# Optimization experiments

Hardware: AMD Instinct MI355X
Metric: run time of the kernel (lower is better)

The kernel has to match this reference:

```python
import jax, jax.numpy as jnp
import numpy as np

N = 10000
IN_DIM = 256
HID = 256
HEADS = 8
NUM_CLASSES = 40
EPS = 1e-5
NEG_SLOPE = 0.2


def gat_conv(x, src, dst, W, a_src, a_dst, bias, concat):
    # x: [N, F_in]; W: [F_in, H*C]; a_src/a_dst: [H, C]
    n = x.shape[0]
    H, C = a_src.shape
    h = (x @ W).reshape(n, H, C)                       # [N,H,C]
    s_src = jnp.einsum('nhc,hc->nh', h, a_src)         # [N,H]
    s_dst = jnp.einsum('nhc,hc->nh', h, a_dst)         # [N,H]
    score = jax.nn.leaky_relu(s_src[src] + s_dst[dst], NEG_SLOPE)  # [E,H]
    m = jax.lax.stop_gradient(jax.ops.segment_max(score, dst, num_segments=n))
    e = jnp.exp(score - m[dst])                        # [E,H]
    denom = jax.ops.segment_sum(e, dst, num_segments=n)
    alpha = e / denom[dst]                             # per-dst edge softmax
    msg = h[src] * alpha[:, :, None]                   # [E,H,C]
    out = jax.ops.segment_sum(msg, dst, num_segments=n)  # [N,H,C]
    out = out.reshape(n, H * C) if concat else out.mean(axis=1)
    return out + bias


def batch_norm(x, gamma, beta):
    mu = x.mean(axis=0)
    var = x.var(axis=0)
    return gamma * (x - mu) * jax.lax.rsqrt(var + EPS) + beta


def setup_inputs() -> dict:
    key = jax.random.key(0)
    ks = jax.random.split(key, 16)
    C0 = HID // HEADS  # 32, concat layer
    x = jax.random.normal(ks[0], (N, IN_DIM), jnp.float32)
    edge_index = jax.random.randint(ks[1], (2, 160000), 0, N, jnp.int32)
    def lin(k, fi, fo):
        return jax.random.normal(k, (fi, fo), jnp.float32) / np.sqrt(fi)
    return {
        'x': x,
        'edge_index': edge_index,
        'W0': lin(ks[2], IN_DIM, HEADS * C0),
        'a_src0': jax.random.normal(ks[3], (HEADS, C0), jnp.float32) * 0.1,
        'a_dst0': jax.random.normal(ks[4], (HEADS, C0), jnp.float32) * 0.1,
        'b0': jnp.zeros((HID,), jnp.float32),
        'g0': jnp.ones((HID,), jnp.float32),
        'be0': jnp.zeros((HID,), jnp.float32),
        'W1': lin(ks[5], HID, HEADS * HID),
        'a_src1': jax.random.normal(ks[6], (HEADS, HID), jnp.float32) * 0.1,
        'a_dst1': jax.random.normal(ks[7], (HEADS, HID), jnp.float32) * 0.1,
        'b1': jnp.zeros((HID,), jnp.float32),
        'g1': jnp.ones((HID,), jnp.float32),
        'be1': jnp.zeros((HID,), jnp.float32),
        'Wc': lin(ks[8], HID, NUM_CLASSES),
        'bc': jnp.zeros((NUM_CLASSES,), jnp.float32),
    }


def reference(x, edge_index, W0, a_src0, a_dst0, b0, g0, be0,
              W1, a_src1, a_dst1, b1, g1, be1, Wc, bc):
    n = x.shape[0]
    loops = jnp.arange(n, dtype=edge_index.dtype)
    src = jnp.concatenate([edge_index[0], loops])  # add_self_loops=True
    dst = jnp.concatenate([edge_index[1], loops])

    # layer 0: concat=True -> [N, 256]
    h = gat_conv(x, src, dst, W0, a_src0, a_dst0, b0, concat=True)
    h = jax.nn.elu(batch_norm(h, g0, be0))
    # i==0: no residual; dropout is identity at eval

    # layer 1 (last): concat=False (mean over heads) -> [N, 256]
    h_in = h
    h = gat_conv(h, src, dst, W1, a_src1, a_dst1, b1, concat=False)
    h = jax.nn.elu(batch_norm(h, g1, be1)) + h_in  # residual for i>0

    return h @ Wc + bc  # logits [N, num_classes]
```

## Files before the change

### kernel.cpp

```cpp
#include <hip/hip_runtime.h>
#include <math.h>

#define NN 10000
#define HEADS 8
#define NCLS 40
#define CHK 64
#define LOG2E 1.4426950408889634f

typedef __attribute__((ext_vector_type(8))) short short8;
typedef __attribute__((ext_vector_type(4))) float floatx4;

static __device__ __forceinline__ short f2bf(float f) {
    unsigned u = __builtin_bit_cast(unsigned, f);
    unsigned r = (u + 0x7fff + ((u >> 16) & 1)) >> 16;
    return (short)r;
}
static __device__ __forceinline__ float bf2f(unsigned short u) {
    unsigned x = ((unsigned)u) << 16;
    return __builtin_bit_cast(float, x);
}
static __device__ __forceinline__ void gl2lds16(const void* g, void* l) {
    __builtin_amdgcn_global_load_lds(
        (const __attribute__((address_space(1))) unsigned int*)g,
        (__attribute__((address_space(3))) unsigned int*)l, 16, 0, 0);
}

__global__ __launch_bounds__(256) void gemm_bf16_w128(
    const short* __restrict__ A, const short* __restrict__ Bt,
    float* __restrict__ C, short* __restrict__ Cbf,
    float* __restrict__ stats, int M, int Nn, int K, float alpha)
{
    __shared__ short As[64 * 64];
    __shared__ short Bs[128 * 64];
    const int tid = threadIdx.x;
    const int w = tid >> 6, L = tid & 63;
    const int quad = L >> 4, lr = L & 15;
    const int col0 = blockIdx.x * 128, row0 = blockIdx.y * 64;

    const int schunk = (L & 7) ^ (L >> 3);
    const int sarow = w * 16 + (L >> 3);
    int ga0 = row0 + sarow;     if (ga0 > M - 1) ga0 = M - 1;
    int ga1 = row0 + sarow + 8; if (ga1 > M - 1) ga1 = M - 1;
    const short* agp0 = A + (size_t)ga0 * K + schunk * 8;
    const short* agp1 = A + (size_t)ga1 * K + schunk * 8;
    short* alp0 = &As[w * 1024];
    short* alp1 = &As[w * 1024 + 512];
    const int sbrow = w * 32 + (L >> 3);
    int gb[4];
    #pragma unroll
    for (int c = 0; c < 4; c++) {
        gb[c] = col0 + sbrow + c * 8;
        if (gb[c] > Nn - 1) gb[c] = Nn - 1;
    }
    const short* bgp0 = Bt + (size_t)gb[0] * K + schunk * 8;
    const short* bgp1 = Bt + (size_t)gb[1] * K + schunk * 8;
    const short* bgp2 = Bt + (size_t)gb[2] * K + schunk * 8;
    const short* bgp3 = Bt + (size_t)gb[3] * K + schunk * 8;
    short* blp0 = &Bs[w * 2048];
    short* blp1 = &Bs[w * 2048 + 512];
    short* blp2 = &Bs[w * 2048 + 1024];
    short* blp3 = &Bs[w * 2048 + 1536];

    floatx4 acc[4][2];
    const floatx4 zf = {0.f, 0.f, 0.f, 0.f};
    #pragma unroll
    for (int i = 0; i < 4; i++)
        #pragma unroll
        for (int j = 0; j < 2; j++) acc[i][j] = zf;

    for (int k0 = 0; k0 < K; k0 += 64) {
        gl2lds16(agp0 + k0, alp0);
        gl2lds16(agp1 + k0, alp1);
        gl2lds16(bgp0 + k0, blp0);
        gl2lds16(bgp1 + k0, blp1);
        gl2lds16(bgp2 + k0, blp2);
        gl2lds16(bgp3 + k0, blp3);
        __syncthreads();
        #pragma unroll
        for (int ks = 0; ks < 2; ks++) {
            const int sl = ((ks * 4 + quad) ^ (lr & 7)) * 8;
            short8 bfr[2];
            #pragma unroll
            for (int j = 0; j < 2; j++)
                bfr[j] = *(const short8*)&Bs[(w * 32 + j * 16 + lr) * 64 + sl];
            #pragma unroll
            for (int i = 0; i < 4; i++) {
                short8 afr = *(const short8*)&As[(i * 16 + lr) * 64 + sl];
                #pragma unroll
                for (int j = 0; j < 2; j++)
                    acc[i][j] = __builtin_amdgcn_mfma_f32_16x16x32_bf16(afr, bfr[j], acc[i][j], 0, 0, 0);
            }
        }
        __syncthreads();
    }
    float s[2] = {0.f, 0.f}, s2[2] = {0.f, 0.f};
    #pragma unroll
    for (int j = 0; j < 2; j++) {
        int ccol = col0 + w * 32 + j * 16 + lr;
        if (ccol >= Nn) continue;
        #pragma unroll
        for (int i = 0; i < 4; i++) {
            #pragma unroll
            for (int r = 0; r < 4; r++) {
                int crow = row0 + i * 16 + quad * 4 + r;
                if (crow < M) {
                    float v = alpha * acc[i][j][r];
                    if (C)   C[(size_t)crow * Nn + ccol] = v;
                    if (Cbf) Cbf[(size_t)crow * Nn + ccol] = f2bf(v);
                    s[j] += v; s2[j] += v * v;
                }
            }
        }
    }
    if (stats) {
        #pragma unroll
        for (int j = 0; j < 2; j++) {
            s[j]  += __shfl_xor(s[j], 16, 64);  s[j]  += __shfl_xor(s[j], 32, 64);
            s2[j] += __shfl_xor(s2[j], 16, 64); s2[j] += __shfl_xor(s2[j], 32, 64);
        }
        if (L < 16) {
            #pragma unroll
            for (int j = 0; j < 2; j++) {
                int ccol = col0 + w * 32 + j * 16 + L;
                if (ccol < Nn) {
                    atomicAdd(&stats[ccol], s[j]);
                    atomicAdd(&stats[256 + ccol], s2[j]);
                }
            }
        }
    }
}

__global__ __launch_bounds__(256) void gemm_bf16_v3(
    const short* __restrict__ A, const short* __restrict__ Bt,
    float* __restrict__ C, const float* __restrict__ bias,
    int M, int Nn, int K, float alpha)
{
    __shared__ short As[64 * 64];
    __shared__ short Bs[64 * 64];
    const int tid = threadIdx.x;
    const int w = tid >> 6, L = tid & 63;
    const int quad = L >> 4, lr = L & 15;
    const int col0 = blockIdx.x * 64, row0 = blockIdx.y * 64;

    const int srow = w * 16 + (L >> 3);
    const int schunk = (L & 7) ^ (L >> 3);
    int ga0 = row0 + srow;     if (ga0 > M - 1)  ga0 = M - 1;
    int ga1 = row0 + srow + 8; if (ga1 > M - 1)  ga1 = M - 1;
    int gb0 = col0 + srow;     if (gb0 > Nn - 1) gb0 = Nn - 1;
    int gb1 = col0 + srow + 8; if (gb1 > Nn - 1) gb1 = Nn - 1;
    const short* agp0 = A + (size_t)ga0 * K + schunk * 8;
    const short* agp1 = A + (size_t)ga1 * K + schunk * 8;
    const short* bgp0 = Bt + (size_t)gb0 * K + schunk * 8;
    const short* bgp1 = Bt + (size_t)gb1 * K + schunk * 8;
    short* alp0 = &As[w * 1024];
    short* alp1 = &As[w * 1024 + 512];
    short* blp0 = &Bs[w * 1024];
    short* blp1 = &Bs[w * 1024 + 512];

    floatx4 acc[4];
    const floatx4 zf = {0.f, 0.f, 0.f, 0.f};
    #pragma unroll
    for (int i = 0; i < 4; i++) acc[i] = zf;

    for (int k0 = 0; k0 < K; k0 += 64) {
        gl2lds16(agp0 + k0, alp0);
        gl2lds16(agp1 + k0, alp1);
        gl2lds16(bgp0 + k0, blp0);
        gl2lds16(bgp1 + k0, blp1);
        __syncthreads();
        #pragma unroll
        for (int ks = 0; ks < 2; ks++) {
            const int sl = ((ks * 4 + quad) ^ (lr & 7)) * 8;
            short8 bfr = *(const short8*)&Bs[(w * 16 + lr) * 64 + sl];
            #pragma unroll
            for (int i = 0; i < 4; i++) {
                short8 afr = *(const short8*)&As[(i * 16 + lr) * 64 + sl];
                acc[i] = __builtin_amdgcn_mfma_f32_16x16x32_bf16(afr, bfr, acc[i], 0, 0, 0);
            }
        }
        __syncthreads();
    }
    const int ccol = col0 + w * 16 + lr;
    if (ccol < Nn) {
        float bv = bias ? bias[ccol] : 0.f;
        #pragma unroll
        for (int i = 0; i < 4; i++) {
            #pragma unroll
            for (int r = 0; r < 4; r++) {
                int crow = row0 + i * 16 + quad * 4 + r;
                if (crow < M) C[(size_t)crow * Nn + ccol] = alpha * acc[i][r] + bv;
            }
        }
    }
}

__global__ __launch_bounds__(1024) void scan_kernel(
    int* counts, int* offsets, int* cursor, int* elist, int n)
{
    const int P = (n + 1023) >> 10;
    __shared__ int wsum[16];
    int tid = threadIdx.x, lane = tid & 63, wid = tid >> 6;
    int base = tid * P;
    int local[16];
    int deg[16];
    int s = 0;
    for (int j = 0; j < P; j++) {
        int i = base + j;
        local[j] = s;
        deg[j] = (i < n) ? counts[i] + 1 : 0;
        s += deg[j];
    }
    int inc = s;
    #pragma unroll
    for (int off = 1; off < 64; off <<= 1) {
        int tv = __shfl_up(inc, off, 64);
        if (lane >= off) inc += tv;
    }
    if (lane == 63) wsum[wid] = inc;
    __syncthreads();
    if (tid < 16) {
        int v = wsum[tid];
        int winc = v;
        #pragma unroll
        for (int off = 1; off < 16; off <<= 1) {
            int tv = __shfl_up(winc, off, 16);
            if (tid >= off) winc += tv;
        }
        wsum[tid] = winc - v;
    }
    __syncthreads();
    int excl = inc - s + wsum[wid];
    for (int j = 0; j < P; j++) {
        int i = base + j;
        if (i < n) {
            int o = excl + local[j];
            counts[i] = deg[j];
            offsets[i] = o;
            elist[o] = i;
            cursor[i] = o + 1;
        }
    }
}

__global__ void scatter_edges_kernel(const int* __restrict__ src, const int* __restrict__ dst,
                                     int* cursor, int* elist, int E) {
    int e = blockIdx.x * 256 + threadIdx.x;
    if (e < E) {
        int d = dst[e];
        int pos = atomicAdd(&cursor[d], 1);
        elist[pos] = src[e];
    }
}

__global__ __launch_bounds__(256) void prep_count(
    const float* __restrict__ x, const float* __restrict__ W0,
    const float* __restrict__ W1, const float* __restrict__ a_src1,
    const float* __restrict__ a_dst1, const float* __restrict__ Wc,
    const int* __restrict__ edst, int E,
    short* __restrict__ xb, short* __restrict__ W0T, float* __restrict__ v1,
    short* __restrict__ W1pT, short* __restrict__ WcT, int* __restrict__ counts)
{
    __shared__ float tile[32][33];
    const int b = blockIdx.x, t = threadIdx.x;
    if (b < 2500) {
        int i = b * 256 + t;
        floatx4 v = ((const floatx4*)x)[i];
        short4 o = {f2bf(v[0]), f2bf(v[1]), f2bf(v[2]), f2bf(v[3])};
        ((short4*)xb)[i] = o;
    } else if (b < 2756) {
        int o = b - 2500;
        W0T[o * 256 + t] = f2bf(W0[t * 256 + o]);
    } else if (b < 2772) {
        int idx = (b - 2756) * 256 + t;
        int f = idx >> 4, j = idx & 15;
        int h = j & 7;
        const float* a = (j < 8) ? a_src1 : a_dst1;
        float s = 0.f;
        for (int c = 0; c < 256; c++)
            s += W1[f * 2048 + h * 256 + c] * a[h * 256 + c];
        v1[idx] = s;
    } else if (b < 3284) {
        int id = b - 2772;
        int h = id >> 6, f0 = ((id >> 3) & 7) * 32, c0 = (id & 7) * 32;
        int tx = t & 31, ty = t >> 5;
        for (int r = ty; r < 32; r += 8)
            tile[r][tx] = W1[(size_t)(f0 + r) * 2048 + h * 256 + c0 + tx];
        __syncthreads();
        for (int r = ty; r < 32; r += 8)
            W1pT[(size_t)(c0 + r) * 2048 + h * 256 + f0 + tx] = f2bf(tile[tx][r]);
    } else if (b < 3324) {
        int o = b - 3284;
        WcT[o * 256 + t] = f2bf(Wc[t * 40 + o]);
    } else {
        int e = (b - 3324) * 256 + t;
        if (e < E) atomicAdd(&counts[edst[e]], 1);
    }
}

__global__ __launch_bounds__(256) void score0_wave(
    const unsigned short* __restrict__ h0b, const float* __restrict__ a_src,
    const float* __restrict__ a_dst, float* __restrict__ s0)
{
    const int wid = threadIdx.x >> 6, L = threadIdx.x & 63;
    const int n = blockIdx.x * 4 + wid;
    ushort4 vv = *(const ushort4*)(h0b + (size_t)n * 256 + 4 * L);
    floatx4 as = *(const floatx4*)(a_src + 4 * L);
    floatx4 ad = *(const floatx4*)(a_dst + 4 * L);
    float v0 = bf2f(vv.x), v1_ = bf2f(vv.y), v2 = bf2f(vv.z), v3 = bf2f(vv.w);
    float ps = v0 * as[0] + v1_ * as[1] + v2 * as[2] + v3 * as[3];
    float pd = v0 * ad[0] + v1_ * ad[1] + v2 * ad[2] + v3 * ad[3];
    #pragma unroll
    for (int off = 1; off < 8; off <<= 1) {
        ps += __shfl_xor(ps, off, 64);
        pd += __shfl_xor(pd, off, 64);
    }
    if ((L & 7) == 0) {
        s0[n * 16 + (L >> 3)] = ps;
        s0[n * 16 + 8 + (L >> 3)] = pd;
    }
}

__global__ __launch_bounds__(256) void agg0_fused(
    const unsigned short* __restrict__ h0b, const float* __restrict__ s0,
    const int* __restrict__ offsets, const int* __restrict__ counts,
    const int* __restrict__ elist, float* __restrict__ out)
{
    __shared__ float pw_s[4][CHK * 8];
    __shared__ int   sn_s[4][CHK];
    const int wid = threadIdx.x >> 6, L = threadIdx.x & 63;
    const int n = blockIdx.x * 4 + wid;
    float* pw = pw_s[wid];
    int*   sw = sn_s[wid];
    const int deg = counts[n], start = offsets[n];
    const int hL = L >> 3;

    floatx4 sda = *(const floatx4*)(s0 + n * 16 + 8);
    floatx4 sdb = *(const floatx4*)(s0 + n * 16 + 12);
    float sd[8] = {sda[0], sda[1], sda[2], sda[3], sdb[0], sdb[1], sdb[2], sdb[3]};
    float lp[8] = {0.f, 0.f, 0.f, 0.f, 0.f, 0.f, 0.f, 0.f};
    float a0 = 0.f, a1 = 0.f, a2 = 0.f, a3 = 0.f;

    for (int e0 = 0; e0 < deg; e0 += CHK) {
        int ch = deg - e0; if (ch > CHK) ch = CHK;
        if (L < ch) {
            int sn = elist[start + e0 + L];
            sw[L] = sn;
            floatx4 ssa = *(const floatx4*)(s0 + sn * 16);
            floatx4 ssb = *(const floatx4*)(s0 + sn * 16 + 4);
            float ss[8] = {ssa[0], ssa[1], ssa[2], ssa[3], ssb[0], ssb[1], ssb[2], ssb[3]};
            float p[8];
            #pragma unroll
            for (int h = 0; h < 8; h++) {
                float v = ss[h] + sd[h];
                v = (v > 0.f) ? v : 0.2f * v;
                p[h] = exp2f(v * LOG2E);
                lp[h] += p[h];
            }
            floatx4 p0 = {p[0], p[1], p[2], p[3]};
            floatx4 p1 = {p[4], p[5], p[6], p[7]};
            *(floatx4*)&pw[L * 8] = p0;
            *(floatx4*)&pw[L * 8 + 4] = p1;
        }
        for (int e = 0; e < ch; e++) {
            float wgt = pw[e * 8 + hL];
            ushort4 vv = *(const ushort4*)(h0b + (size_t)sw[e] * 256 + 4 * L);
            a0 += wgt * bf2f(vv.x);
            a1 += wgt * bf2f(vv.y);
            a2 += wgt * bf2f(vv.z);
            a3 += wgt * bf2f(vv.w);
        }
    }
    #pragma unroll
    for (int off = 1; off < 64; off <<= 1)
        #pragma unroll
        for (int h = 0; h < 8; h++)
            lp[h] += __shfl_xor(lp[h], off, 64);
    float inv = 1.f / lp[hL];
    floatx4 o = {a0 * inv, a1 * inv, a2 * inv, a3 * inv};
    *(floatx4*)(out + (size_t)n * 256 + 4 * L) = o;
}

__global__ __launch_bounds__(256) void agg1_half(
    const unsigned short* __restrict__ hb, const float* __restrict__ s1,
    const int* __restrict__ offsets, const int* __restrict__ counts,
    const int* __restrict__ elist, short* __restrict__ aggout)
{
    __shared__ float pw_s[4][CHK * 4];
    __shared__ int   sn_s[4][CHK];
    const int wid = threadIdx.x >> 6, L = threadIdx.x & 63;
    const int n = blockIdx.x * 2 + (wid >> 1);
    const int hg = wid & 1;
    float* pw = pw_s[wid];
    int*   sw = sn_s[wid];
    const int deg = counts[n], start = offsets[n];

    floatx4 sd4 = *(const floatx4*)(s1 + n * 16 + 8 + hg * 4);
    float lp[4] = {0.f, 0.f, 0.f, 0.f};
    float acc[4][4];
    #pragma unroll
    for (int h = 0; h < 4; h++)
        #pragma unroll
        for (int f = 0; f < 4; f++) acc[h][f] = 0.f;

    for (int e0 = 0; e0 < deg; e0 += CHK) {
        int ch = deg - e0; if (ch > CHK) ch = CHK;
        if (L < ch) {
            int sn = elist[start + e0 + L];
            sw[L] = sn;
            floatx4 ss4 = *(const floatx4*)(s1 + sn * 16 + hg * 4);
            floatx4 p4;
            #pragma unroll
            for (int h = 0; h < 4; h++) {
                float v = ss4[h] + sd4[h];
                v = (v > 0.f) ? v : 0.2f * v;
                float p = exp2f(v * LOG2E);
                p4[h] = p;
                lp[h] += p;
            }
            *(floatx4*)&pw[L * 4] = p4;
        }
        for (int e = 0; e < ch; e++) {
            floatx4 pv = *(const floatx4*)&pw[e * 4];
            ushort4 vv = *(const ushort4*)(hb + (size_t)sw[e] * 256 + 4 * L);
            float v0 = bf2f(vv.x), v1_ = bf2f(vv.y), v2 = bf2f(vv.z), v3 = bf2f(vv.w);
            #pragma unroll
            for (int h = 0; h < 4; h++) {
                acc[h][0] += pv[h] * v0;
                acc[h][1] += pv[h] * v1_;
                acc[h][2] += pv[h] * v2;
                acc[h][3] += pv[h] * v3;
            }
        }
    }
    #pragma unroll
    for (int off = 1; off < 64; off <<= 1)
        #pragma unroll
        for (int h = 0; h < 4; h++)
            lp[h] += __shfl_xor(lp[h], off, 64);
    #pragma unroll
    for (int h = 0; h < 4; h++) {
        float inv = 1.f / lp[h];
        short4 o = {f2bf(acc[h][0] * inv), f2bf(acc[h][1] * inv),
                    f2bf(acc[h][2] * inv), f2bf(acc[h][3] * inv)};
        *(short4*)(aggout + (size_t)n * 2048 + (hg * 4 + h) * 256 + 4 * L) = o;
    }
}

__global__ __launch_bounds__(256) void bn_stats_kernel(const float* __restrict__ x, float* stats, int n) {
    int t = threadIdx.x;
    float s = 0.f, s2 = 0.f;
    for (int r = blockIdx.x; r < n; r += gridDim.x) {
        float v = x[(size_t)r * 256 + t];
        s += v; s2 += v * v;
    }
    atomicAdd(&stats[t], s);
    atomicAdd(&stats[256 + t], s2);
}

__global__ __launch_bounds__(256) void bnapply_score1(
    const float* __restrict__ xg, const float* __restrict__ stats,
    const float* __restrict__ g, const float* __restrict__ be,
    const float* __restrict__ v1, short* __restrict__ hactb, float* __restrict__ s1)
{
    __shared__ float row[256];
    __shared__ float part[16][17];
    const int n = blockIdx.x, t = threadIdx.x;
    const float invN = 1.0f / NN;
    float mu = stats[t] * invN;
    float var = stats[256 + t] * invN - mu * mu;
    float v = g[t] * (xg[(size_t)n * 256 + t] - mu) * rsqrtf(var + 1e-5f) + be[t];
    v = (v > 0.f) ? v : (expf(v) - 1.f);
    hactb[(size_t)n * 256 + t] = f2bf(v);
    row[t] = v;
    __syncthreads();
    int j = t & 15, f0 = t >> 4;
    float p = 0.f;
    #pragma unroll
    for (int k = 0; k < 16; k++)
        p += row[f0 * 16 + k] * v1[(f0 * 16 + k) * 16 + j];
    part[f0][j] = p;
    __syncthreads();
    if (t < 16) {
        float s = 0.f;
        #pragma unroll
        for (int k = 0; k < 16; k++) s += part[k][t];
        s1[n * 16 + t] = s;
    }
}

__global__ __launch_bounds__(256) void bn_apply_kernel(
    const float* __restrict__ x, const float* __restrict__ stats,
    const float* __restrict__ g, const float* __restrict__ be,
    const unsigned short* __restrict__ resid, short* __restrict__ ybf, int total)
{
    int i = blockIdx.x * 256 + threadIdx.x;
    if (i >= total) return;
    int c = i & 255;
    const float invN = 1.0f / NN;
    float mu = stats[c] * invN;
    float var = stats[256 + c] * invN - mu * mu;
    float v = g[c] * (x[i] - mu) * rsqrtf(var + 1e-5f) + be[c];
    v = (v > 0.f) ? v : (expf(v) - 1.f);
    v += bf2f(resid[i]);
    ybf[i] = f2bf(v);
}

extern "C" void kernel_launch(void* const* d_in, const int* in_sizes, int n_in,
                              void* d_out, int out_size, void* d_ws, size_t ws_size,
                              hipStream_t stream) {
    const float* x      = (const float*)d_in[0];
    const int*   eidx   = (const int*)d_in[1];
    const float* W0     = (const float*)d_in[2];
    const float* a_src0 = (const float*)d_in[3];
    const float* a_dst0 = (const float*)d_in[4];
    const float* g0     = (const float*)d_in[6];
    const float* be0    = (const float*)d_in[7];
    const float* W1     = (const float*)d_in[8];
    const float* a_src1 = (const float*)d_in[9];
    const float* a_dst1 = (const float*)d_in[10];
    const float* g1     = (const float*)d_in[12];
    const float* be1    = (const float*)d_in[13];
    const float* Wc     = (const float*)d_in[14];
    const float* bc     = (const float*)d_in[15];
    float* out = (float*)d_out;

    const int E = in_sizes[1] / 2;
    const int* esrc = eidx;
    const int* edst = eidx + E;

    char* ws = (char*)d_ws;
    size_t off = 0;
    auto alloc = [&](size_t bytes) {
        void* p = ws + off;
        off += (bytes + 255) & ~(size_t)255;
        return p;
    };
    float* stats   = (float*)alloc(1024 * 4);
    int*   counts  = (int*)alloc(NN * 4);
    float* out1    = (float*)alloc((size_t)NN * 256 * 4);
    short* h0b     = (short*)alloc((size_t)NN * 256 * 2);
    short* xb      = (short*)alloc((size_t)NN * 256 * 2);
    float* s0      = (float*)alloc((size_t)NN * 16 * 4);
    float* s1      = (float*)alloc((size_t)NN * 16 * 4);
    float* v1      = (float*)alloc(4096 * 4);
    float* h_gat0  = (float*)alloc((size_t)NN * 256 * 4);
    short* hactb   = (short*)alloc((size_t)NN * 256 * 2);
    short* agg1bf  = (short*)alloc((size_t)NN * 2048 * 2);
    short* W0T     = (short*)alloc((size_t)256 * 256 * 2);
    short* W1pT    = (short*)alloc((size_t)256 * 2048 * 2);
    short* WcT     = (short*)alloc((size_t)64 * 256 * 2);
    short* hfinbf  = (short*)alloc((size_t)NN * 256 * 2);
    int* offsets   = (int*)alloc((NN + 16) * 4);
    int* cursor    = (int*)alloc(NN * 4);
    int* elist     = (int*)alloc((size_t)(E + NN) * 4);

    float* stats0 = stats;
    float* stats1 = stats + 512;

    hipMemsetAsync(stats, 0, 1024 * 4 + NN * 4, stream);

    const int cntBlocks = (E + 255) / 256;
    prep_count<<<3324 + cntBlocks, 256, 0, stream>>>(
        x, W0, W1, a_src1, a_dst1, Wc, edst, E,
        xb, W0T, v1, W1pT, WcT, counts);

    scan_kernel<<<1, 1024, 0, stream>>>(counts, offsets, cursor, elist, NN);
    scatter_edges_kernel<<<cntBlocks, 256, 0, stream>>>(esrc, edst, cursor, elist, E);

    {
        dim3 grid(2, (NN + 63) / 64);
        gemm_bf16_w128<<<grid, 256, 0, stream>>>(xb, W0T, nullptr, h0b, nullptr,
                                                 NN, 256, 256, 1.0f);
    }
    score0_wave<<<NN / 4, 256, 0, stream>>>(
        (const unsigned short*)h0b, a_src0, a_dst0, s0);
    agg0_fused<<<NN / 4, 256, 0, stream>>>(
        (const unsigned short*)h0b, s0, offsets, counts, elist, h_gat0);
    bn_stats_kernel<<<256, 256, 0, stream>>>(h_gat0, stats0, NN);
    bnapply_score1<<<NN, 256, 0, stream>>>(h_gat0, stats0, g0, be0, v1, hactb, s1);

    agg1_half<<<NN / 2, 256, 0, stream>>>(
        (const unsigned short*)hactb, s1, offsets, counts, elist, agg1bf);
    {
        dim3 grid(2, (NN + 63) / 64);
        gemm_bf16_w128<<<grid, 256, 0, stream>>>(agg1bf, W1pT, out1, nullptr, stats1,
                                                 NN, 256, 2048, 0.125f);
    }
    bn_apply_kernel<<<(NN * 256 + 255) / 256, 256, 0, stream>>>(
        out1, stats1, g1, be1, (const unsigned short*)hactb, hfinbf, NN * 256);

    {
        dim3 grid(1, (NN + 63) / 64);
        gemm_bf16_v3<<<grid, 256, 0, stream>>>(hfinbf, WcT, out, bc,
                                               NN, NCLS, 256, 1.0f);
    }
}
```

Baseline: 277.0 us.

## Fuse edge scatter, layer-0 scores, and BN into GEMMs; widen layer-1 aggregation

The edge scatter now runs as extra blocks of the first GEMM launch, and the layer-0 attention scores are computed in that GEMM's epilogue instead of a separate pass. The final batchnorm, ELU and residual step is folded into the classifier GEMM's A-operand load, which removes the bf16 intermediate buffer and one kernel. Layer-1 aggregation now handles all 8 heads per wave, so each gathered source row is read once instead of twice, at the cost of more registers. The GEMM grid is also swizzled into a 1D order, and the BN stats kernel uses vectorized loads with fewer blocks.

```diff
diff --git a/kernel.cpp b/kernel.cpp
--- a/kernel.cpp
+++ b/kernel.cpp
@@ -8,6 +8,7 @@
 #define LOG2E 1.4426950408889634f
 
 typedef __attribute__((ext_vector_type(8))) short short8;
+typedef __attribute__((ext_vector_type(8))) unsigned short ushort8v;
 typedef __attribute__((ext_vector_type(4))) float floatx4;
 
 static __device__ __forceinline__ short f2bf(float f) {
@@ -28,14 +29,33 @@
 __global__ __launch_bounds__(256) void gemm_bf16_w128(
     const short* __restrict__ A, const short* __restrict__ Bt,
     float* __restrict__ C, short* __restrict__ Cbf,
-    float* __restrict__ stats, int M, int Nn, int K, float alpha)
+    float* __restrict__ stats,
+    const float* __restrict__ asrc, const float* __restrict__ adst,
+    float* __restrict__ s0,
+    const int* __restrict__ esrc, const int* __restrict__ edst,
+    int* __restrict__ cursor, int* __restrict__ elist, int E,
+    int gemmBlocks, int gridY,
+    int M, int Nn, int K, float alpha)
 {
+    if ((int)blockIdx.x >= gemmBlocks) {
+        int e = ((int)blockIdx.x - gemmBlocks) * 256 + threadIdx.x;
+        if (e < E) {
+            int dn = edst[e];
+            int pos = atomicAdd(&cursor[dn], 1);
+            elist[pos] = esrc[e];
+        }
+        return;
+    }
     __shared__ short As[64 * 64];
     __shared__ short Bs[128 * 64];
     const int tid = threadIdx.x;
     const int w = tid >> 6, L = tid & 63;
     const int quad = L >> 4, lr = L & 15;
-    const int col0 = blockIdx.x * 128, row0 = blockIdx.y * 64;
+    const int d = blockIdx.x;
+    const int by = (d >> 4) * 8 + (d & 7);
+    const int bx = (d >> 3) & 1;
+    if (by >= gridY) return;
+    const int col0 = bx * 128, row0 = by * 64;
 
     const int schunk = (L & 7) ^ (L >> 3);
     const int sarow = w * 16 + (L >> 3);
@@ -129,32 +149,63 @@
             }
         }
     }
-}
-
-__global__ __launch_bounds__(256) void gemm_bf16_v3(
-    const short* __restrict__ A, const short* __restrict__ Bt,
-    float* __restrict__ C, const float* __restrict__ bias,
-    int M, int Nn, int K, float alpha)
+    if (s0) {
+        const int head = bx * 4 + w;
+        float as0 = asrc[col0 + w * 32 + lr];
+        float as1 = asrc[col0 + w * 32 + 16 + lr];
+        float ad0 = adst[col0 + w * 32 + lr];
+        float ad1 = adst[col0 + w * 32 + 16 + lr];
+        #pragma unroll
+        for (int i = 0; i < 4; i++) {
+            #pragma unroll
+            for (int r = 0; r < 4; r++) {
+                float ps = acc[i][0][r] * as0 + acc[i][1][r] * as1;
+                float pd = acc[i][0][r] * ad0 + acc[i][1][r] * ad1;
+                #pragma unroll
+                for (int off = 1; off < 16; off <<= 1) {
+                    ps += __shfl_xor(ps, off, 64);
+                    pd += __shfl_xor(pd, off, 64);
+                }
+                if (lr == 0) {
+                    int crow = row0 + i * 16 + quad * 4 + r;
+                    if (crow < M) {
+                        s0[crow * 16 + head] = alpha * ps;
+                        s0[crow * 16 + 8 + head] = alpha * pd;
+                    }
+                }
+            }
+        }
+    }
+}
+
+__global__ __launch_bounds__(256) void classifier_fused(
+    const float* __restrict__ X, const float* __restrict__ stats,
+    const float* __restrict__ g, const float* __restrict__ be,
+    const unsigned short* __restrict__ resid,
+    const short* __restrict__ Bt, float* __restrict__ C,
+    const float* __restrict__ bias, int M, int Nn, int K)
 {
     __shared__ short As[64 * 64];
     __shared__ short Bs[64 * 64];
     const int tid = threadIdx.x;
     const int w = tid >> 6, L = tid & 63;
     const int quad = L >> 4, lr = L & 15;
-    const int col0 = blockIdx.x * 64, row0 = blockIdx.y * 64;
+    const int row0 = blockIdx.x * 64;
 
     const int srow = w * 16 + (L >> 3);
     const int schunk = (L & 7) ^ (L >> 3);
     int ga0 = row0 + srow;     if (ga0 > M - 1)  ga0 = M - 1;
     int ga1 = row0 + srow + 8; if (ga1 > M - 1)  ga1 = M - 1;
-    int gb0 = col0 + srow;     if (gb0 > Nn - 1) gb0 = Nn - 1;
-    int gb1 = col0 + srow + 8; if (gb1 > Nn - 1) gb1 = Nn - 1;
-    const short* agp0 = A + (size_t)ga0 * K + schunk * 8;
-    const short* agp1 = A + (size_t)ga1 * K + schunk * 8;
+    int gb0 = srow;     if (gb0 > Nn - 1) gb0 = Nn - 1;
+    int gb1 = srow + 8; if (gb1 > Nn - 1) gb1 = Nn - 1;
+    const float* xg0 = X + (size_t)ga0 * K + schunk * 8;
+    const float* xg1 = X + (size_t)ga1 * K + schunk * 8;
+    const unsigned short* rg0 = resid + (size_t)ga0 * K + schunk * 8;
+    const unsigned short* rg1 = resid + (size_t)ga1 * K + schunk * 8;
     const short* bgp0 = Bt + (size_t)gb0 * K + schunk * 8;
     const short* bgp1 = Bt + (size_t)gb1 * K + schunk * 8;
-    short* alp0 = &As[w * 1024];
-    short* alp1 = &As[w * 1024 + 512];
+    short* alw0 = &As[w * 1024 + L * 8];
+    short* alw1 = &As[w * 1024 + 512 + L * 8];
     short* blp0 = &Bs[w * 1024];
     short* blp1 = &Bs[w * 1024 + 512];
 
@@ -162,12 +213,58 @@
     const floatx4 zf = {0.f, 0.f, 0.f, 0.f};
     #pragma unroll
     for (int i = 0; i < 4; i++) acc[i] = zf;
+    const float invN = 1.0f / NN;
 
     for (int k0 = 0; k0 < K; k0 += 64) {
-        gl2lds16(agp0 + k0, alp0);
-        gl2lds16(agp1 + k0, alp1);
         gl2lds16(bgp0 + k0, blp0);
         gl2lds16(bgp1 + k0, blp1);
+        const int c = schunk * 8 + k0;
+        floatx4 mu_a = *(const floatx4*)(stats + c);
+        floatx4 mu_b = *(const floatx4*)(stats + c + 4);
+        floatx4 sq_a = *(const floatx4*)(stats + 256 + c);
+        floatx4 sq_b = *(const floatx4*)(stats + 256 + c + 4);
+        floatx4 g_a  = *(const floatx4*)(g + c);
+        floatx4 g_b  = *(const floatx4*)(g + c + 4);
+        floatx4 be_a = *(const floatx4*)(be + c);
+        floatx4 be_b = *(const floatx4*)(be + c + 4);
+        float scl[8], sh[8];
+        #pragma unroll
+        for (int q = 0; q < 8; q++) {
+            float m  = (q < 4 ? mu_a[q & 3] : mu_b[q & 3]) * invN;
+            float sq = (q < 4 ? sq_a[q & 3] : sq_b[q & 3]) * invN;
+            float gv = (q < 4 ? g_a[q & 3]  : g_b[q & 3]);
+            float bv = (q < 4 ? be_a[q & 3] : be_b[q & 3]);
+            float rs = rsqrtf(sq - m * m + 1e-5f) * gv;
+            scl[q] = rs; sh[q] = bv - m * rs;
+        }
+        {
+            floatx4 xa = *(const floatx4*)(xg0 + k0);
+            floatx4 xb2 = *(const floatx4*)(xg0 + k0 + 4);
+            ushort8v rv = *(const ushort8v*)(rg0 + k0);
+            short8 av;
+            #pragma unroll
+            for (int q = 0; q < 8; q++) {
+                float v = (q < 4 ? xa[q & 3] : xb2[q & 3]) * scl[q] + sh[q];
+                v = (v > 0.f) ? v : (expf(v) - 1.f);
+                v += bf2f(rv[q]);
+                av[q] = f2bf(v);
+            }
+            *(short8*)alw0 = av;
+        }
+        {
+            floatx4 xa = *(const floatx4*)(xg1 + k0);
+            floatx4 xb2 = *(const floatx4*)(xg1 + k0 + 4);
+            ushort8v rv = *(const ushort8v*)(rg1 + k0);
+            short8 av;
+            #pragma unroll
+            for (int q = 0; q < 8; q++) {
+                float v = (q < 4 ? xa[q & 3] : xb2[q & 3]) * scl[q] + sh[q];
+                v = (v > 0.f) ? v : (expf(v) - 1.f);
+                v += bf2f(rv[q]);
+                av[q] = f2bf(v);
+            }
+            *(short8*)alw1 = av;
+        }
         __syncthreads();
         #pragma unroll
         for (int ks = 0; ks < 2; ks++) {
@@ -181,7 +278,7 @@
         }
         __syncthreads();
     }
-    const int ccol = col0 + w * 16 + lr;
+    const int ccol = w * 16 + lr;
     if (ccol < Nn) {
         float bv = bias ? bias[ccol] : 0.f;
         #pragma unroll
@@ -189,7 +286,7 @@
             #pragma unroll
             for (int r = 0; r < 4; r++) {
                 int crow = row0 + i * 16 + quad * 4 + r;
-                if (crow < M) C[(size_t)crow * Nn + ccol] = alpha * acc[i][r] + bv;
+                if (crow < M) C[(size_t)crow * Nn + ccol] = acc[i][r] + bv;
             }
         }
     }
@@ -240,16 +337,6 @@
             elist[o] = i;
             cursor[i] = o + 1;
         }
-    }
-}
-
-__global__ void scatter_edges_kernel(const int* __restrict__ src, const int* __restrict__ dst,
-                                     int* cursor, int* elist, int E) {
-    int e = blockIdx.x * 256 + threadIdx.x;
-    if (e < E) {
-        int d = dst[e];
-        int pos = atomicAdd(&cursor[d], 1);
-        elist[pos] = src[e];
     }
 }
 
@@ -298,29 +385,6 @@
     }
 }
 
-__global__ __launch_bounds__(256) void score0_wave(
-    const unsigned short* __restrict__ h0b, const float* __restrict__ a_src,
-    const float* __restrict__ a_dst, float* __restrict__ s0)
-{
-    const int wid = threadIdx.x >> 6, L = threadIdx.x & 63;
-    const int n = blockIdx.x * 4 + wid;
-    ushort4 vv = *(const ushort4*)(h0b + (size_t)n * 256 + 4 * L);
-    floatx4 as = *(const floatx4*)(a_src + 4 * L);
-    floatx4 ad = *(const floatx4*)(a_dst + 4 * L);
-    float v0 = bf2f(vv.x), v1_ = bf2f(vv.y), v2 = bf2f(vv.z), v3 = bf2f(vv.w);
-    float ps = v0 * as[0] + v1_ * as[1] + v2 * as[2] + v3 * as[3];
-    float pd = v0 * ad[0] + v1_ * ad[1] + v2 * ad[2] + v3 * ad[3];
-    #pragma unroll
-    for (int off = 1; off < 8; off <<= 1) {
-        ps += __shfl_xor(ps, off, 64);
-        pd += __shfl_xor(pd, off, 64);
-    }
-    if ((L & 7) == 0) {
-        s0[n * 16 + (L >> 3)] = ps;
-        s0[n * 16 + 8 + (L >> 3)] = pd;
-    }
-}
-
 __global__ __launch_bounds__(256) void agg0_fused(
     const unsigned short* __restrict__ h0b, const float* __restrict__ s0,
     const int* __restrict__ offsets, const int* __restrict__ counts,
@@ -381,25 +445,26 @@
     *(floatx4*)(out + (size_t)n * 256 + 4 * L) = o;
 }
 
-__global__ __launch_bounds__(256) void agg1_half(
+__global__ __launch_bounds__(256) void agg1_full(
     const unsigned short* __restrict__ hb, const float* __restrict__ s1,
     const int* __restrict__ offsets, const int* __restrict__ counts,
     const int* __restrict__ elist, short* __restrict__ aggout)
 {
-    __shared__ float pw_s[4][CHK * 4];
+    __shared__ float pw_s[4][CHK * 8];
     __shared__ int   sn_s[4][CHK];
     const int wid = threadIdx.x >> 6, L = threadIdx.x & 63;
-    const int n = blockIdx.x * 2 + (wid >> 1);
-    const int hg = wid & 1;
+    const int n = blockIdx.x * 4 + wid;
     float* pw = pw_s[wid];
     int*   sw = sn_s[wid];
     const int deg = counts[n], start = offsets[n];
 
-    floatx4 sd4 = *(const floatx4*)(s1 + n * 16 + 8 + hg * 4);
-    float lp[4] = {0.f, 0.f, 0.f, 0.f};
-    float acc[4][4];
-    #pragma unroll
-    for (int h = 0; h < 4; h++)
+    floatx4 sda = *(const floatx4*)(s1 + n * 16 + 8);
+    floatx4 sdb = *(const floatx4*)(s1 + n * 16 + 12);
+    float sd[8] = {sda[0], sda[1], sda[2], sda[3], sdb[0], sdb[1], sdb[2], sdb[3]};
+    float lp[8] = {0.f, 0.f, 0.f, 0.f, 0.f, 0.f, 0.f, 0.f};
+    float acc[8][4];
+    #pragma unroll
+    for (int h = 0; h < 8; h++)
         #pragma unroll
         for (int f = 0; f < 4; f++) acc[h][f] = 0.f;
 
@@ -408,54 +473,63 @@
         if (L < ch) {
             int sn = elist[start + e0 + L];
             sw[L] = sn;
-            floatx4 ss4 = *(const floatx4*)(s1 + sn * 16 + hg * 4);
-            floatx4 p4;
-            #pragma unroll
-            for (int h = 0; h < 4; h++) {
-                float v = ss4[h] + sd4[h];
+            floatx4 ssa = *(const floatx4*)(s1 + sn * 16);
+            floatx4 ssb = *(const floatx4*)(s1 + sn * 16 + 4);
+            float ss[8] = {ssa[0], ssa[1], ssa[2], ssa[3], ssb[0], ssb[1], ssb[2], ssb[3]};
+            float p[8];
+            #pragma unroll
+            for (int h = 0; h < 8; h++) {
+                float v = ss[h] + sd[h];
                 v = (v > 0.f) ? v : 0.2f * v;
-                float p = exp2f(v * LOG2E);
-                p4[h] = p;
-                lp[h] += p;
-            }
-            *(floatx4*)&pw[L * 4] = p4;
+                p[h] = exp2f(v * LOG2E);
+                lp[h] += p[h];
+            }
+            floatx4 p0 = {p[0], p[1], p[2], p[3]};
+            floatx4 p1 = {p[4], p[5], p[6], p[7]};
+            *(floatx4*)&pw[L * 8] = p0;
+            *(floatx4*)&pw[L * 8 + 4] = p1;
         }
         for (int e = 0; e < ch; e++) {
-            floatx4 pv = *(const floatx4*)&pw[e * 4];
+            floatx4 p0 = *(const floatx4*)&pw[e * 8];
+            floatx4 p1 = *(const floatx4*)&pw[e * 8 + 4];
             ushort4 vv = *(const ushort4*)(hb + (size_t)sw[e] * 256 + 4 * L);
             float v0 = bf2f(vv.x), v1_ = bf2f(vv.y), v2 = bf2f(vv.z), v3 = bf2f(vv.w);
             #pragma unroll
             for (int h = 0; h < 4; h++) {
-                acc[h][0] += pv[h] * v0;
-                acc[h][1] += pv[h] * v1_;
-                acc[h][2] += pv[h] * v2;
-                acc[h][3] += pv[h] * v3;
+                acc[h][0] += p0[h] * v0;     acc[h][1] += p0[h] * v1_;
+                acc[h][2] += p0[h] * v2;     acc[h][3] += p0[h] * v3;
+                acc[h + 4][0] += p1[h] * v0; acc[h + 4][1] += p1[h] * v1_;
+                acc[h + 4][2] += p1[h] * v2; acc[h + 4][3] += p1[h] * v3;
             }
         }
     }
     #pragma unroll
     for (int off = 1; off < 64; off <<= 1)
         #pragma unroll
-        for (int h = 0; h < 4; h++)
+        for (int h = 0; h < 8; h++)
             lp[h] += __shfl_xor(lp[h], off, 64);
     #pragma unroll
-    for (int h = 0; h < 4; h++) {
+    for (int h = 0; h < 8; h++) {
         float inv = 1.f / lp[h];
         short4 o = {f2bf(acc[h][0] * inv), f2bf(acc[h][1] * inv),
                     f2bf(acc[h][2] * inv), f2bf(acc[h][3] * inv)};
-        *(short4*)(aggout + (size_t)n * 2048 + (hg * 4 + h) * 256 + 4 * L) = o;
+        *(short4*)(aggout + (size_t)n * 2048 + h * 256 + 4 * L) = o;
     }
 }
 
 __global__ __launch_bounds__(256) void bn_stats_kernel(const float* __restrict__ x, float* stats, int n) {
     int t = threadIdx.x;
-    float s = 0.f, s2 = 0.f;
-    for (int r = blockIdx.x; r < n; r += gridDim.x) {
-        float v = x[(size_t)r * 256 + t];
+    int sub = t >> 6, c4 = (t & 63) * 4;
+    floatx4 s = {0.f, 0.f, 0.f, 0.f}, s2 = {0.f, 0.f, 0.f, 0.f};
+    for (int r = blockIdx.x * 4 + sub; r < n; r += gridDim.x * 4) {
+        floatx4 v = *(const floatx4*)(x + (size_t)r * 256 + c4);
         s += v; s2 += v * v;
     }
-    atomicAdd(&stats[t], s);
-    atomicAdd(&stats[256 + t], s2);
+    #pragma unroll
+    for (int k = 0; k < 4; k++) {
+        atomicAdd(&stats[c4 + k], s[k]);
+        atomicAdd(&stats[256 + c4 + k], s2[k]);
+    }
 }
 
 __global__ __launch_bounds__(256) void bnapply_score1(
@@ -487,23 +561,6 @@
         for (int k = 0; k < 16; k++) s += part[k][t];
         s1[n * 16 + t] = s;
     }
-}
-
-__global__ __launch_bounds__(256) void bn_apply_kernel(
-    const float* __restrict__ x, const float* __restrict__ stats,
-    const float* __restrict__ g, const float* __restrict__ be,
-    const unsigned short* __restrict__ resid, short* __restrict__ ybf, int total)
-{
-    int i = blockIdx.x * 256 + threadIdx.x;
-    if (i >= total) return;
-    int c = i & 255;
-    const float invN = 1.0f / NN;
-    float mu = stats[c] * invN;
-    float var = stats[256 + c] * invN - mu * mu;
-    float v = g[c] * (x[i] - mu) * rsqrtf(var + 1e-5f) + be[c];
-    v = (v > 0.f) ? v : (expf(v) - 1.f);
-    v += bf2f(resid[i]);
-    ybf[i] = f2bf(v);
 }
 
 extern "C" void kernel_launch(void* const* d_in, const int* in_sizes, int n_in,
@@ -550,7 +607,6 @@
     short* W0T     = (short*)alloc((size_t)256 * 256 * 2);
     short* W1pT    = (short*)alloc((size_t)256 * 2048 * 2);
     short* WcT     = (short*)alloc((size_t)64 * 256 * 2);
-    short* hfinbf  = (short*)alloc((size_t)NN * 256 * 2);
     int* offsets   = (int*)alloc((NN + 16) * 4);
     int* cursor    = (int*)alloc(NN * 4);
     int* elist     = (int*)alloc((size_t)(E + NN) * 4);
@@ -566,33 +622,30 @@
         xb, W0T, v1, W1pT, WcT, counts);
 
     scan_kernel<<<1, 1024, 0, stream>>>(counts, offsets, cursor, elist, NN);
-    scatter_edges_kernel<<<cntBlocks, 256, 0, stream>>>(esrc, edst, cursor, elist, E);
-
-    {
-        dim3 grid(2, (NN + 63) / 64);
-        gemm_bf16_w128<<<grid, 256, 0, stream>>>(xb, W0T, nullptr, h0b, nullptr,
-                                                 NN, 256, 256, 1.0f);
-    }
-    score0_wave<<<NN / 4, 256, 0, stream>>>(
-        (const unsigned short*)h0b, a_src0, a_dst0, s0);
+
+    const int gy = (NN + 63) / 64;
+    const int gB = 16 * ((gy + 7) / 8);
+
+    gemm_bf16_w128<<<gB + cntBlocks, 256, 0, stream>>>(
+        xb, W0T, nullptr, h0b, nullptr,
+        a_src0, a_dst0, s0,
+        esrc, edst, cursor, elist, E,
+        gB, gy, NN, 256, 256, 1.0f);
+
     agg0_fused<<<NN / 4, 256, 0, stream>>>(
         (const unsigned short*)h0b, s0, offsets, counts, elist, h_gat0);
-    bn_stats_kernel<<<256, 256, 0, stream>>>(h_gat0, stats0, NN);
+    bn_stats_kernel<<<64, 256, 0, stream>>>(h_gat0, stats0, NN);
     bnapply_score1<<<NN, 256, 0, stream>>>(h_gat0, stats0, g0, be0, v1, hactb, s1);
 
-    agg1_half<<<NN / 2, 256, 0, stream>>>(
+    agg1_full<<<NN / 4, 256, 0, stream>>>(
         (const unsigned short*)hactb, s1, offsets, counts, elist, agg1bf);
-    {
-        dim3 grid(2, (NN + 63) / 64);
-        gemm_bf16_w128<<<grid, 256, 0, stream>>>(agg1bf, W1pT, out1, nullptr, stats1,
-                                                 NN, 256, 2048, 0.125f);
-    }
-    bn_apply_kernel<<<(NN * 256 + 255) / 256, 256, 0, stream>>>(
-        out1, stats1, g1, be1, (const unsigned short*)hactb, hfinbf, NN * 256);
-
-    {
-        dim3 grid(1, (NN + 63) / 64);
-        gemm_bf16_v3<<<grid, 256, 0, stream>>>(hfinbf, WcT, out, bc,
-                                               NN, NCLS, 256, 1.0f);
-    }
-}
+    gemm_bf16_w128<<<gB, 256, 0, stream>>>(
+        agg1bf, W1pT, out1, nullptr, stats1,
+        nullptr, nullptr, nullptr,
+        nullptr, nullptr, nullptr, nullptr, 0,
+        gB, gy, NN, 256, 2048, 0.125f);
+
+    classifier_fused<<<gy, 256, 0, stream>>>(
+        out1, stats1, g1, be1, (const unsigned short*)hactb,
+        WcT, out, bc, NN, NCLS, 256);
+}
```

Measured after the change: 285.0 us. 2.9% more time.
